# Kernel optimization log

Hardware: AMD Instinct MI355X
Metric: run time of the kernel (lower is better)

The kernel has to match this reference:

```python
import jax, jax.numpy as jnp
import numpy as np

H = 8          # num_heads
D_MODEL = 512  # hidden_dim
HEAD_DIM = D_MODEL // H
SCALE = HEAD_DIM ** -0.5
N = 4096
NUM_GRAPHS = 32
NEG_INF = jnp.float32(-jnp.inf)


def setup_inputs() -> dict:
    key = jax.random.key(0)
    ks = jax.random.split(key, 12)
    w_std = D_MODEL ** -0.5  # ~ torch Linear init scale
    inp = {
        "x": jax.random.normal(ks[0], (N, D_MODEL), jnp.float32),
        "attention_bias": jax.random.normal(ks[1], (H, N, N), jnp.float32),
        "batch": jnp.sort(jax.random.randint(ks[2], (N,), 0, NUM_GRAPHS)),
        "Wq": jax.random.normal(ks[3], (D_MODEL, D_MODEL), jnp.float32) * w_std,
        "bq": jax.random.normal(ks[4], (D_MODEL,), jnp.float32) * w_std,
        "Wk": jax.random.normal(ks[5], (D_MODEL, D_MODEL), jnp.float32) * w_std,
        "bk": jax.random.normal(ks[6], (D_MODEL,), jnp.float32) * w_std,
        "Wv": jax.random.normal(ks[7], (D_MODEL, D_MODEL), jnp.float32) * w_std,
        "bv": jax.random.normal(ks[8], (D_MODEL,), jnp.float32) * w_std,
        "Wo": jax.random.normal(ks[9], (D_MODEL, D_MODEL), jnp.float32) * w_std,
        "bo": jax.random.normal(ks[10], (D_MODEL,), jnp.float32) * w_std,
    }
    return inp


def reference(x, attention_bias, batch, Wq, bq, Wk, bk, Wv, bv, Wo, bo):
    n = x.shape[0]
    # projections (torch Linear: y = x @ W.T + b)
    q = (x @ Wq.T + bq).reshape(n, H, HEAD_DIM)
    k = (x @ Wk.T + bk).reshape(n, H, HEAD_DIM)
    v = (x @ Wv.T + bv).reshape(n, H, HEAD_DIM)
    # scores [H, N, N] with relative-PE bias
    attn = jnp.einsum("nhd,mhd->hnm", q, k) * SCALE + attention_bias
    # batch mask: attend only within the same graph
    batch_mask = batch[:, None] != batch[None, :]  # [N, N], True = masked
    attn = jnp.where(batch_mask[None, :, :], NEG_INF, attn)
    attn = jax.nn.softmax(attn, axis=-1)
    attn = jnp.nan_to_num(attn, nan=0.0)
    # dropout is identity in eval / dropout=0.0
    out = jnp.einsum("hnm,mhd->nhd", attn, v).reshape(n, D_MODEL)
    out = out @ Wo.T + bo
    return out
```

## Files before the change

### kernel.cpp

```cpp
#include <hip/hip_runtime.h>

#define NTOK 4096
#define DMODEL 512
#define NHEAD 8
#define HDIM 64
#define KDIM 512

typedef __bf16 bf16x8 __attribute__((ext_vector_type(8)));
typedef float f32x4 __attribute__((ext_vector_type(4)));
typedef unsigned short u16x8 __attribute__((ext_vector_type(8)));
typedef unsigned short u16x4 __attribute__((ext_vector_type(4)));

#define NEGINF (-__builtin_inff())

__device__ __forceinline__ f32x4 mfma16(bf16x8 a, bf16x8 b, f32x4 c) {
  return __builtin_amdgcn_mfma_f32_16x16x32_bf16(a, b, c, 0, 0, 0);
}

__device__ __forceinline__ unsigned short f2bf(float f) {
  unsigned u = __builtin_bit_cast(unsigned, f);
  u += 0x7FFFu + ((u >> 16) & 1u);
  return (unsigned short)(u >> 16);
}

__device__ __forceinline__ void gload_lds16(const void* g, void* l) {
  __builtin_amdgcn_global_load_lds(
      (const __attribute__((address_space(1))) void*)g,
      (__attribute__((address_space(3))) void*)l, 16, 0, 0);
}

__device__ __forceinline__ int lbound(const int* __restrict__ b, int val) {
  int lo = 0, hi = NTOK;
  while (lo < hi) {
    int mid = (lo + hi) >> 1;
    if (b[mid] < val) lo = mid + 1; else hi = mid;
  }
  return lo;
}

__global__ void convert_kernel(const float* __restrict__ x,
                               const float* __restrict__ Wq, const float* __restrict__ bq,
                               const float* __restrict__ Wk, const float* __restrict__ bk,
                               const float* __restrict__ Wv, const float* __restrict__ bv,
                               const float* __restrict__ Wo,
                               const int* __restrict__ batch,
                               unsigned short* __restrict__ xb,
                               unsigned short* __restrict__ wqkv,
                               unsigned short* __restrict__ wo,
                               float* __restrict__ bqkv,
                               int* __restrict__ qrange) {
  const int XV = NTOK * DMODEL / 4;
  const int WV = DMODEL * DMODEL / 4;
  const int total = XV + 4 * WV + 1536 / 4;
  for (int i = blockIdx.x * blockDim.x + threadIdx.x; i < total;
       i += gridDim.x * blockDim.x) {
    if (i < XV) {
      float4 v = ((const float4*)x)[i];
      u16x4 pk = {f2bf(v.x), f2bf(v.y), f2bf(v.z), f2bf(v.w)};
      *(u16x4*)(xb + (size_t)i * 4) = pk;
    } else if (i < XV + 3 * WV) {
      int j = i - XV;
      const float* W; float sc; int jj;
      if (j < WV)          { W = Wq; sc = 0.125f; jj = j; }
      else if (j < 2 * WV) { W = Wk; sc = 1.0f;  jj = j - WV; }
      else                 { W = Wv; sc = 1.0f;  jj = j - 2 * WV; }
      float4 v = ((const float4*)W)[jj];
      u16x4 pk = {f2bf(v.x * sc), f2bf(v.y * sc), f2bf(v.z * sc), f2bf(v.w * sc)};
      *(u16x4*)(wqkv + (size_t)j * 4) = pk;
    } else if (i < XV + 4 * WV) {
      int j = i - XV - 3 * WV;
      float4 v = ((const float4*)Wo)[j];
      u16x4 pk = {f2bf(v.x), f2bf(v.y), f2bf(v.z), f2bf(v.w)};
      *(u16x4*)(wo + (size_t)j * 4) = pk;
    } else {
      int j = (i - XV - 4 * WV) * 4;
      #pragma unroll
      for (int t = 0; t < 4; ++t) {
        int e = j + t;
        float v = (e < 512) ? bq[e] * 0.125f
                 : (e < 1024 ? bk[e - 512] : bv[e - 1024]);
        bqkv[e] = v;
      }
    }
  }
  if (blockIdx.x == 0 && threadIdx.x < 256) {
    int q0 = threadIdx.x * 16;
    int blo = batch[q0];
    int bhi = batch[q0 + 15];
    qrange[threadIdx.x * 2]     = lbound(batch, blo) >> 6;
    qrange[threadIdx.x * 2 + 1] = (lbound(batch, bhi + 1) + 63) >> 6;
  }
}

template <int MODE>
__global__ __launch_bounds__(256) void gemm_kernel(
    const unsigned short* __restrict__ A,
    const unsigned short* __restrict__ B,
    const float* __restrict__ biasv,
    float* __restrict__ outf,
    unsigned short* __restrict__ qb,
    unsigned short* __restrict__ kb,
    unsigned short* __restrict__ vt) {
  __shared__ __align__(16) unsigned short lds[(128 + 64) * 64];
  unsigned short* ldsA = lds;
  unsigned short* ldsB = lds + 128 * 64;
  const int tid = threadIdx.x;
  const int lane = tid & 63;
  const int wv = tid >> 6;
  const int wm = wv >> 1, wn = wv & 1;
  const int r16 = lane & 15, g4 = lane >> 4;
  const int mt = blockIdx.x, nt = blockIdx.y;

  f32x4 acc[4][2];
  #pragma unroll
  for (int i = 0; i < 4; ++i)
    #pragma unroll
    for (int j = 0; j < 2; ++j)
      acc[i][j] = (f32x4){0.f, 0.f, 0.f, 0.f};

  const int srow = tid >> 3;
  const int scolb = (tid & 7) << 4;

  for (int kt = 0; kt < KDIM / 64; ++kt) {
    __syncthreads();
    #pragma unroll
    for (int i = 0; i < 4; ++i) {
      int row = i * 32 + srow;
      int colu = scolb ^ ((row & 7) << 4);
      const unsigned short* ga =
          A + (size_t)(mt * 128 + row) * KDIM + kt * 64 + (colu >> 1);
      gload_lds16(ga, (char*)ldsA + i * 4096 + wv * 1024);
    }
    #pragma unroll
    for (int i = 0; i < 2; ++i) {
      int row = i * 32 + srow;
      int colu = scolb ^ ((row & 7) << 4);
      const unsigned short* gb =
          B + (size_t)(nt * 64 + row) * KDIM + kt * 64 + (colu >> 1);
      gload_lds16(gb, (char*)ldsB + i * 4096 + wv * 1024);
    }
    __syncthreads();
    #pragma unroll
    for (int ks = 0; ks < 2; ++ks) {
      bf16x8 af[4], bfr[2];
      #pragma unroll
      for (int f = 0; f < 4; ++f) {
        int ra = wm * 64 + f * 16 + r16;
        af[f] = *(const bf16x8*)((const char*)ldsA + ra * 128 +
                                 ((ks * 64 + g4 * 16) ^ ((ra & 7) << 4)));
      }
      #pragma unroll
      for (int f = 0; f < 2; ++f) {
        int rb = wn * 32 + f * 16 + r16;
        bfr[f] = *(const bf16x8*)((const char*)ldsB + rb * 128 +
                                  ((ks * 64 + g4 * 16) ^ ((rb & 7) << 4)));
      }
      #pragma unroll
      for (int fm = 0; fm < 4; ++fm)
        #pragma unroll
        for (int fn = 0; fn < 2; ++fn)
          acc[fm][fn] = mfma16(af[fm], bfr[fn], acc[fm][fn]);
    }
  }

  #pragma unroll
  for (int fm = 0; fm < 4; ++fm) {
    #pragma unroll
    for (int fn = 0; fn < 2; ++fn) {
      int mb = mt * 128 + wm * 64 + fm * 16 + g4 * 4;
      int n = nt * 64 + wn * 32 + fn * 16 + r16;
      float bv = biasv[n];
      if (MODE == 1) {
        #pragma unroll
        for (int r = 0; r < 4; ++r)
          outf[(size_t)(mb + r) * DMODEL + n] = acc[fm][fn][r] + bv;
      } else {
        if (n < 512) {
          #pragma unroll
          for (int r = 0; r < 4; ++r)
            qb[(size_t)(mb + r) * DMODEL + n] = f2bf(acc[fm][fn][r] + bv);
        } else if (n < 1024) {
          int nn = n - 512;
          #pragma unroll
          for (int r = 0; r < 4; ++r)
            kb[(size_t)(mb + r) * DMODEL + nn] = f2bf(acc[fm][fn][r] + bv);
        } else {
          int nn = n - 1024;
          u16x4 pk;
          #pragma unroll
          for (int r = 0; r < 4; ++r) pk[r] = f2bf(acc[fm][fn][r] + bv);
          *(u16x4*)(vt + (size_t)nn * NTOK + mb) = pk;
        }
      }
    }
  }
}

__global__ __launch_bounds__(64) void attn_kernel(
    const unsigned short* __restrict__ qb,
    const unsigned short* __restrict__ kb,
    const unsigned short* __restrict__ vt,
    const float* __restrict__ bias,
    const int* __restrict__ batch,
    const int* __restrict__ qrange,
    unsigned short* __restrict__ ao) {
  __shared__ __align__(16) unsigned short pl[16 * 72];
  const int lane = threadIdx.x & 63;
  const int r16 = lane & 15, g4 = lane >> 4;
  const int h = blockIdx.x & 7;
  const int qt = blockIdx.x >> 3;
  const int qrow0 = qt * 16;
  const int hoff = h * HDIM;

  const unsigned short* qrow = qb + (size_t)(qrow0 + r16) * DMODEL + hoff + g4 * 8;
  bf16x8 qa0 = *(const bf16x8*)qrow;
  bf16x8 qa1 = *(const bf16x8*)(qrow + 32);

  int qbt[4];
  const float* bprow[4];
  const float* bh = bias + (size_t)h * NTOK * NTOK;
  #pragma unroll
  for (int r = 0; r < 4; ++r) {
    qbt[r] = batch[qrow0 + g4 * 4 + r];
    bprow[r] = bh + (size_t)(qrow0 + g4 * 4 + r) * NTOK;
  }

  const int tile0 = qrange[qt * 2];
  const int tile1 = qrange[qt * 2 + 1];

  float m_r[4] = {NEGINF, NEGINF, NEGINF, NEGINF};
  float l_r[4] = {0.f, 0.f, 0.f, 0.f};
  f32x4 o[4];
  #pragma unroll
  for (int d = 0; d < 4; ++d) o[d] = (f32x4){0.f, 0.f, 0.f, 0.f};

#define PREFETCH_KB(T, K0, K1, BV, KBT)                                      \
  {                                                                          \
    int kvb_ = (T) << 6;                                                     \
    _Pragma("unroll") for (int c = 0; c < 4; ++c) {                          \
      const unsigned short* kp =                                             \
          kb + (size_t)(kvb_ + c * 16 + r16) * DMODEL + hoff + g4 * 8;       \
      K0[c] = *(const bf16x8*)kp;                                            \
      K1[c] = *(const bf16x8*)(kp + 32);                                     \
    }                                                                        \
    _Pragma("unroll") for (int c = 0; c < 4; ++c) {                          \
      KBT[c] = batch[kvb_ + c * 16 + r16];                                   \
      _Pragma("unroll") for (int r = 0; r < 4; ++r)                          \
        BV[c][r] = bprow[r][kvb_ + c * 16 + r16];                            \
    }                                                                        \
  }

#define TILE_STEP(T, K0C, K1C, BVC, KBTC, K0N, K1N, BVN, KBTN)               \
  {                                                                          \
    int kvb = (T) << 6;                                                      \
    f32x4 s[4];                                                              \
    _Pragma("unroll") for (int c = 0; c < 4; ++c) {                          \
      f32x4 z = (f32x4){0.f, 0.f, 0.f, 0.f};                                 \
      z = mfma16(qa0, K0C[c], z);                                            \
      z = mfma16(qa1, K1C[c], z);                                            \
      s[c] = z;                                                              \
    }                                                                        \
        \
    bf16x8 v0[4], v1[4];                                                     \
    _Pragma("unroll") for (int d = 0; d < 4; ++d) {                          \
      const unsigned short* vp =                                             \
          vt + (size_t)(hoff + d * 16 + r16) * NTOK + kvb + g4 * 8;          \
      v0[d] = *(const bf16x8*)vp;                                            \
      v1[d] = *(const bf16x8*)(vp + 32);                                     \
    }                                                                        \
     \
    {                                                                        \
      int tn_ = ((T) + 1 < tile1) ? (T) + 1 : (T);                           \
      PREFETCH_KB(tn_, K0N, K1N, BVN, KBTN);                                 \
    }                                                                        \
    _Pragma("unroll") for (int c = 0; c < 4; ++c)                            \
      _Pragma("unroll") for (int r = 0; r < 4; ++r)                          \
        s[c][r] = (qbt[r] == KBTC[c]) ? (s[c][r] + BVC[c][r]) : NEGINF;      \
    float scl[4];                                                            \
    _Pragma("unroll") for (int r = 0; r < 4; ++r) {                          \
      float tm = fmaxf(fmaxf(s[0][r], s[1][r]), fmaxf(s[2][r], s[3][r]));    \
      tm = fmaxf(tm, __shfl_xor(tm, 1));                                     \
      tm = fmaxf(tm, __shfl_xor(tm, 2));                                     \
      tm = fmaxf(tm, __shfl_xor(tm, 4));                                     \
      tm = fmaxf(tm, __shfl_xor(tm, 8));                                     \
      float mn = fmaxf(m_r[r], tm);                                          \
      bool dead = (mn == NEGINF);                                            \
      scl[r] = dead ? 1.0f : __expf(m_r[r] - mn);                            \
      m_r[r] = mn;                                                           \
      float rs = 0.f;                                                        \
      _Pragma("unroll") for (int c = 0; c < 4; ++c) {                        \
        float p = dead ? 0.0f : __expf(s[c][r] - mn);                        \
        s[c][r] = p;                                                         \
        rs += p;                                                             \
      }                                                                      \
      rs += __shfl_xor(rs, 1);                                               \
      rs += __shfl_xor(rs, 2);                                               \
      rs += __shfl_xor(rs, 4);                                               \
      rs += __shfl_xor(rs, 8);                                               \
      l_r[r] = l_r[r] * scl[r] + rs;                                         \
    }                                                                        \
    _Pragma("unroll") for (int c = 0; c < 4; ++c)                            \
      _Pragma("unroll") for (int r = 0; r < 4; ++r)                          \
        pl[(g4 * 4 + r) * 72 + c * 16 + r16] = f2bf(s[c][r]);                \
    asm volatile("" ::: "memory");                                           \
    u16x8 pr0 = *(const u16x8*)(pl + r16 * 72 + g4 * 8);                     \
    u16x8 pr1 = *(const u16x8*)(pl + r16 * 72 + 32 + g4 * 8);                \
    bf16x8 pa0 = __builtin_bit_cast(bf16x8, pr0);                            \
    bf16x8 pa1 = __builtin_bit_cast(bf16x8, pr1);                            \
    _Pragma("unroll") for (int d = 0; d < 4; ++d) {                          \
      _Pragma("unroll") for (int r = 0; r < 4; ++r) o[d][r] *= scl[r];       \
    }                                                                        \
    _Pragma("unroll") for (int d = 0; d < 4; ++d) {                          \
      o[d] = mfma16(pa0, v0[d], o[d]);                                       \
      o[d] = mfma16(pa1, v1[d], o[d]);                                       \
    }                                                                        \
  }

  bf16x8 ka0[4], ka1[4], kc0[4], kc1[4];
  float bva[4][4], bvb[4][4];
  int kta[4], ktb[4];
  PREFETCH_KB(tile0, ka0, ka1, bva, kta);
  int t = tile0;
  while (true) {
    TILE_STEP(t, ka0, ka1, bva, kta, kc0, kc1, bvb, ktb);
    if (++t >= tile1) break;
    TILE_STEP(t, kc0, kc1, bvb, ktb, ka0, ka1, bva, kta);
    if (++t >= tile1) break;
  }

  #pragma unroll
  for (int r = 0; r < 4; ++r) {
    float inv = (l_r[r] > 0.f) ? 1.0f / l_r[r] : 0.0f;
    #pragma unroll
    for (int d = 0; d < 4; ++d)
      ao[(size_t)(qrow0 + g4 * 4 + r) * DMODEL + hoff + d * 16 + r16] =
          f2bf(o[d][r] * inv);
  }
#undef PREFETCH_KB
#undef TILE_STEP
}

extern "C" void kernel_launch(void* const* d_in, const int* in_sizes, int n_in,
                              void* d_out, int out_size, void* d_ws, size_t ws_size,
                              hipStream_t stream) {
  const float* x  = (const float*)d_in[0];
  const float* ab = (const float*)d_in[1];
  const int* batch = (const int*)d_in[2];
  const float* Wq = (const float*)d_in[3];
  const float* bq = (const float*)d_in[4];
  const float* Wk = (const float*)d_in[5];
  const float* bk = (const float*)d_in[6];
  const float* Wv = (const float*)d_in[7];
  const float* bv = (const float*)d_in[8];
  const float* Wo = (const float*)d_in[9];
  const float* bo = (const float*)d_in[10];
  float* out = (float*)d_out;

  char* ws = (char*)d_ws;
  const size_t MB = 1024 * 1024;
  unsigned short* xb   = (unsigned short*)(ws);
  unsigned short* qb   = (unsigned short*)(ws + 4 * MB);
  unsigned short* kb   = (unsigned short*)(ws + 8 * MB);
  unsigned short* vt   = (unsigned short*)(ws + 12 * MB);
  unsigned short* aout = (unsigned short*)(ws + 16 * MB);
  unsigned short* wqkv = (unsigned short*)(ws + 20 * MB);
  unsigned short* wo   = (unsigned short*)(ws + 22 * MB);
  float* bqkv          = (float*)(ws + 23 * MB);
  int* qrange          = (int*)(ws + 23 * MB + 65536);

  convert_kernel<<<dim3(1024), dim3(256), 0, stream>>>(
      x, Wq, bq, Wk, bk, Wv, bv, Wo, batch, xb, wqkv, wo, bqkv, qrange);

  gemm_kernel<0><<<dim3(32, 24), dim3(256), 0, stream>>>(
      xb, wqkv, bqkv, nullptr, qb, kb, vt);

  attn_kernel<<<dim3(2048), dim3(64), 0, stream>>>(
      qb, kb, vt, ab, batch, qrange, aout);

  gemm_kernel<1><<<dim3(32, 8), dim3(256), 0, stream>>>(
      aout, wo, bo, out, nullptr, nullptr, nullptr);
}
```

Baseline: 54.73 us.

## Triple-buffer GEMM LDS staging with async prefetch; cache batch in shared memory

The projection GEMM now uses three LDS buffers and issues global-to-LDS loads two k-tiles ahead. Explicit vmcnt waits and a single barrier per iteration replace the two full syncthreads around each load/compute step, so memory latency can overlap MFMA work. LDS use per block triples, which may lower occupancy. Separately, the qrange binary searches in the convert kernel now read the batch array from shared memory instead of global memory.

```diff
diff --git a/kernel.cpp b/kernel.cpp
--- a/kernel.cpp
+++ b/kernel.cpp
@@ -5,6 +5,7 @@
 #define NHEAD 8
 #define HDIM 64
 #define KDIM 512
+#define KITER (KDIM / 64)
 
 typedef __bf16 bf16x8 __attribute__((ext_vector_type(8)));
 typedef float f32x4 __attribute__((ext_vector_type(4)));
@@ -27,15 +28,6 @@
   __builtin_amdgcn_global_load_lds(
       (const __attribute__((address_space(1))) void*)g,
       (__attribute__((address_space(3))) void*)l, 16, 0, 0);
-}
-
-__device__ __forceinline__ int lbound(const int* __restrict__ b, int val) {
-  int lo = 0, hi = NTOK;
-  while (lo < hi) {
-    int mid = (lo + hi) >> 1;
-    if (b[mid] < val) lo = mid + 1; else hi = mid;
-  }
-  return lo;
 }
 
 __global__ void convert_kernel(const float* __restrict__ x,
@@ -49,6 +41,10 @@
                                unsigned short* __restrict__ wo,
                                float* __restrict__ bqkv,
                                int* __restrict__ qrange) {
+  __shared__ int bsh[NTOK];
+  if (blockIdx.x == 0) {
+    for (int i = threadIdx.x; i < NTOK; i += 256) bsh[i] = batch[i];
+  }
   const int XV = NTOK * DMODEL / 4;
   const int WV = DMODEL * DMODEL / 4;
   const int total = XV + 4 * WV + 1536 / 4;
@@ -83,15 +79,24 @@
       }
     }
   }
-  if (blockIdx.x == 0 && threadIdx.x < 256) {
-    int q0 = threadIdx.x * 16;
-    int blo = batch[q0];
-    int bhi = batch[q0 + 15];
-    qrange[threadIdx.x * 2]     = lbound(batch, blo) >> 6;
-    qrange[threadIdx.x * 2 + 1] = (lbound(batch, bhi + 1) + 63) >> 6;
-  }
-}
-
+  if (blockIdx.x == 0) {
+    __syncthreads();
+    if (threadIdx.x < 256) {
+      int q0 = threadIdx.x * 16;
+      int blo = bsh[q0];
+      int bhi = bsh[q0 + 15];
+      int lo = 0, hi = NTOK;
+      while (lo < hi) { int m = (lo + hi) >> 1; if (bsh[m] < blo) lo = m + 1; else hi = m; }
+      qrange[threadIdx.x * 2] = lo >> 6;
+      lo = 0; hi = NTOK;
+      while (lo < hi) { int m = (lo + hi) >> 1; if (bsh[m] < bhi + 1) lo = m + 1; else hi = m; }
+      qrange[threadIdx.x * 2 + 1] = (lo + 63) >> 6;
+    }
+  }
+}
+
+#define BUFE (192 * 64)
+#define BUFB (BUFE * 2)
 template <int MODE>
 __global__ __launch_bounds__(256) void gemm_kernel(
     const unsigned short* __restrict__ A,
@@ -101,9 +106,7 @@
     unsigned short* __restrict__ qb,
     unsigned short* __restrict__ kb,
     unsigned short* __restrict__ vt) {
-  __shared__ __align__(16) unsigned short lds[(128 + 64) * 64];
-  unsigned short* ldsA = lds;
-  unsigned short* ldsB = lds + 128 * 64;
+  __shared__ __align__(16) unsigned short lds[3 * BUFE];
   const int tid = threadIdx.x;
   const int lane = tid & 63;
   const int wv = tid >> 6;
@@ -121,47 +124,65 @@
   const int srow = tid >> 3;
   const int scolb = (tid & 7) << 4;
 
-  for (int kt = 0; kt < KDIM / 64; ++kt) {
-    __syncthreads();
-    #pragma unroll
-    for (int i = 0; i < 4; ++i) {
-      int row = i * 32 + srow;
-      int colu = scolb ^ ((row & 7) << 4);
-      const unsigned short* ga =
-          A + (size_t)(mt * 128 + row) * KDIM + kt * 64 + (colu >> 1);
-      gload_lds16(ga, (char*)ldsA + i * 4096 + wv * 1024);
+#define STAGE(KT, BI)                                                        \
+  {                                                                          \
+    char* bA = (char*)lds + (BI) * BUFB;                                     \
+    char* bB = bA + 128 * 128;                                               \
+    _Pragma("unroll") for (int i = 0; i < 4; ++i) {                          \
+      int row = i * 32 + srow;                                               \
+      int cu_ = scolb ^ ((row & 7) << 4);                                    \
+      gload_lds16(A + (size_t)(mt * 128 + row) * KDIM + (KT) * 64 + (cu_ >> 1), \
+                  bA + i * 4096 + wv * 1024);                                \
+    }                                                                        \
+    _Pragma("unroll") for (int i = 0; i < 2; ++i) {                          \
+      int row = i * 32 + srow;                                               \
+      int cu_ = scolb ^ ((row & 7) << 4);                                    \
+      gload_lds16(B + (size_t)(nt * 64 + row) * KDIM + (KT) * 64 + (cu_ >> 1), \
+                  bB + i * 4096 + wv * 1024);                                \
+    }                                                                        \
+  }
+
+#define COMPUTE(BI)                                                          \
+  {                                                                          \
+    const char* base = (const char*)lds + (BI) * BUFB;                       \
+    _Pragma("unroll") for (int ks = 0; ks < 2; ++ks) {                       \
+      bf16x8 af[4], bfr[2];                                                  \
+      _Pragma("unroll") for (int f = 0; f < 4; ++f) {                        \
+        int ra = wm * 64 + f * 16 + r16;                                     \
+        af[f] = *(const bf16x8*)(base + ra * 128 +                           \
+                                 ((ks * 64 + g4 * 16) ^ ((ra & 7) << 4)));   \
+      }                                                                      \
+      _Pragma("unroll") for (int f = 0; f < 2; ++f) {                        \
+        int rb = wn * 32 + f * 16 + r16;                                     \
+        bfr[f] = *(const bf16x8*)(base + 128 * 128 + rb * 128 +              \
+                                  ((ks * 64 + g4 * 16) ^ ((rb & 7) << 4)));  \
+      }                                                                      \
+      _Pragma("unroll") for (int fm = 0; fm < 4; ++fm)                       \
+        _Pragma("unroll") for (int fn = 0; fn < 2; ++fn)                     \
+          acc[fm][fn] = mfma16(af[fm], bfr[fn], acc[fm][fn]);                \
+    }                                                                        \
+  }
+
+  STAGE(0, 0);
+  STAGE(1, 1);
+  int cur = 0;
+  #pragma unroll
+  for (int kt = 0; kt < KITER; ++kt) {
+    if (kt < KITER - 1) {
+      asm volatile("s_waitcnt vmcnt(6)" ::: "memory");
+    } else {
+      asm volatile("s_waitcnt vmcnt(0)" ::: "memory");
     }
-    #pragma unroll
-    for (int i = 0; i < 2; ++i) {
-      int row = i * 32 + srow;
-      int colu = scolb ^ ((row & 7) << 4);
-      const unsigned short* gb =
-          B + (size_t)(nt * 64 + row) * KDIM + kt * 64 + (colu >> 1);
-      gload_lds16(gb, (char*)ldsB + i * 4096 + wv * 1024);
+    __builtin_amdgcn_s_barrier();
+    if (kt + 2 < KITER) {
+      int bi = cur ? cur - 1 : 2;
+      STAGE(kt + 2, bi);
     }
-    __syncthreads();
-    #pragma unroll
-    for (int ks = 0; ks < 2; ++ks) {
-      bf16x8 af[4], bfr[2];
-      #pragma unroll
-      for (int f = 0; f < 4; ++f) {
-        int ra = wm * 64 + f * 16 + r16;
-        af[f] = *(const bf16x8*)((const char*)ldsA + ra * 128 +
-                                 ((ks * 64 + g4 * 16) ^ ((ra & 7) << 4)));
-      }
-      #pragma unroll
-      for (int f = 0; f < 2; ++f) {
-        int rb = wn * 32 + f * 16 + r16;
-        bfr[f] = *(const bf16x8*)((const char*)ldsB + rb * 128 +
-                                  ((ks * 64 + g4 * 16) ^ ((rb & 7) << 4)));
-      }
-      #pragma unroll
-      for (int fm = 0; fm < 4; ++fm)
-        #pragma unroll
-        for (int fn = 0; fn < 2; ++fn)
-          acc[fm][fn] = mfma16(af[fm], bfr[fn], acc[fm][fn]);
-    }
-  }
+    COMPUTE(cur);
+    cur = (cur == 2) ? 0 : cur + 1;
+  }
+#undef STAGE
+#undef COMPUTE
 
   #pragma unroll
   for (int fm = 0; fm < 4; ++fm) {
```

New measurement: 54.11 us. About the same (-1.1%).
